# Kernel optimization log

Measured on AMD Instinct MI355X. Metric: run time of the kernel, lower is better.

## Reference

```python
import jax, jax.numpy as jnp
import numpy as np
from functools import partial

B, T, C, L, H, V = 2, 1024, 1024, 4, 16, 50257
HD = C // H
EPS = 1e-5


def setup_inputs() -> dict:
    key = jax.random.key(0)
    ks = jax.random.split(key, 12)
    s = 0.02
    inp = {
        'idx': jax.random.randint(ks[0], (B, T), 0, V),
        'wte': jax.random.normal(ks[1], (V, C), jnp.float32) * s,
        'wpe': jax.random.normal(ks[2], (T, C), jnp.float32) * s,
        'ln1_w': jnp.ones((L, C), jnp.float32),
        'ln1_b': jnp.zeros((L, C), jnp.float32),
        'attn_w': jax.random.normal(ks[3], (L, 3 * C, C), jnp.float32) * s,
        'attn_b': jnp.zeros((L, 3 * C), jnp.float32),
        'proj_w': jax.random.normal(ks[4], (L, C, C), jnp.float32) * s,
        'proj_b': jnp.zeros((L, C), jnp.float32),
        'ln2_w': jnp.ones((L, C), jnp.float32),
        'ln2_b': jnp.zeros((L, C), jnp.float32),
        'fc_w': jax.random.normal(ks[5], (L, 4 * C, C), jnp.float32) * s,
        'fc_b': jnp.zeros((L, 4 * C), jnp.float32),
        'fc2_w': jax.random.normal(ks[6], (L, C, 4 * C), jnp.float32) * s,
        'fc2_b': jnp.zeros((L, C), jnp.float32),
        'lnf_w': jnp.ones((C,), jnp.float32),
        'lnf_b': jnp.zeros((C,), jnp.float32),
    }
    return inp


def layer_norm(x, w, b):
    m = jnp.mean(x, axis=-1, keepdims=True)
    v = jnp.mean(jnp.square(x - m), axis=-1, keepdims=True)
    return (x - m) * jax.lax.rsqrt(v + EPS) * w + b


def block(x, p):
    (l1w, l1b, aw, ab, pw, pb, l2w, l2b, fw, fb, f2w, f2b) = p
    h = layer_norm(x, l1w, l1b)
    qkv = h @ aw.T + ab  # [B,T,3C]
    q, k, v = jnp.split(qkv, 3, axis=-1)
    q = q.reshape(B, T, H, HD).transpose(0, 2, 1, 3)
    k = k.reshape(B, T, H, HD).transpose(0, 2, 1, 3)
    v = v.reshape(B, T, H, HD).transpose(0, 2, 1, 3)
    # NOTE: source calls masked_fill without assignment -> causal mask is a
    # no-op; faithful reference uses UNMASKED full attention.
    scores = jnp.einsum('bhqd,bhkd->bhqk', q, k) / np.sqrt(HD).astype(np.float32)
    att = jax.nn.softmax(scores, axis=-1)
    o = jnp.einsum('bhqk,bhkd->bhqd', att, v)
    o = o.transpose(0, 2, 1, 3).reshape(B, T, C)
    x = x + (o @ pw.T + pb)
    h2 = layer_norm(x, l2w, l2b)
    h2 = jax.nn.gelu(h2 @ fw.T + fb, approximate=False)
    x = x + (h2 @ f2w.T + f2b)
    return x


def reference(idx, wte, wpe, ln1_w, ln1_b, attn_w, attn_b, proj_w, proj_b,
              ln2_w, ln2_b, fc_w, fc_b, fc2_w, fc2_b, lnf_w, lnf_b):
    x = wte[idx] + wpe[jnp.arange(T)][None, :, :]  # [B,T,C]
    params = (ln1_w, ln1_b, attn_w, attn_b, proj_w, proj_b,
              ln2_w, ln2_b, fc_w, fc_b, fc2_w, fc2_b)
    x, _ = jax.lax.scan(lambda c, p: (block(c, p), None), x, params)
    x = layer_norm(x, lnf_w, lnf_b)
    logits_last = x[:, -1] @ wte.T  # tied lm_head, only last position
    return logits_last
```

## Files before the change

kernel.cpp:

```cpp
#include <hip/hip_runtime.h>
#include <hip/hip_bf16.h>


constexpr int NB = 2;
constexpr int NT = 1024;
constexpr int NC = 1024;
constexpr int NLAYER = 4;
constexpr int NH = 16;
constexpr int DH = 64;
constexpr int NV = 50257;
constexpr int C3 = 3 * NC;
constexpr int C4 = 4 * NC;

typedef __attribute__((ext_vector_type(8))) short bf16x8;
typedef __attribute__((ext_vector_type(4))) float f32x4;
typedef __attribute__((ext_vector_type(4))) short s16x4;

__device__ inline short f2b(float x) {
  union { __hip_bfloat16 h; short s; } u;
  u.h = __float2bfloat16(x);
  return u.s;
}

__device__ inline bf16x8 cvt8(float4 a, float4 b) {
  bf16x8 r;
  r[0] = f2b(a.x); r[1] = f2b(a.y); r[2] = f2b(a.z); r[3] = f2b(a.w);
  r[4] = f2b(b.x); r[5] = f2b(b.y); r[6] = f2b(b.z); r[7] = f2b(b.w);
  return r;
}

__device__ inline void load_lds16(const short* gp, short* lp) {
  __builtin_amdgcn_global_load_lds(
      (const __attribute__((address_space(1))) void*)gp,
      (__attribute__((address_space(3))) void*)lp, 16, 0, 0);
}

__global__ __launch_bounds__(256) void cvt4_kernel(
    const float* __restrict__ s0, const float* __restrict__ s1,
    const float* __restrict__ s2, const float* __restrict__ s3,
    short* __restrict__ d0, short* __restrict__ d1,
    short* __restrict__ d2, short* __restrict__ d3,
    int n0, int n1, int n2, int n3) {
  int total = n0 + n1 + n2 + n3;
  int stride = gridDim.x * 256;
  for (int i = blockIdx.x * 256 + threadIdx.x; i < total; i += stride) {
    const float* s; short* d; int j = i;
    if (j < n0) { s = s0; d = d0; }
    else if ((j -= n0) < n1) { s = s1; d = d1; }
    else if ((j -= n1) < n2) { s = s2; d = d2; }
    else { j -= n2; s = s3; d = d3; }
    float4 v = reinterpret_cast<const float4*>(s)[j];
    s16x4 o;
    o[0] = f2b(v.x); o[1] = f2b(v.y); o[2] = f2b(v.z); o[3] = f2b(v.w);
    reinterpret_cast<s16x4*>(d)[j] = o;
  }
}

__global__ void embed_kernel(const int* __restrict__ idx,
                             const float* __restrict__ wte,
                             const float* __restrict__ wpe,
                             float* __restrict__ x) {
  int row = blockIdx.x;
  int t = row & (NT - 1);
  int id = idx[row];
  const float4* wr = reinterpret_cast<const float4*>(wte + (size_t)id * NC);
  const float4* pr = reinterpret_cast<const float4*>(wpe + (size_t)t * NC);
  float4* xr = reinterpret_cast<float4*>(x + (size_t)row * NC);
  int i = threadIdx.x;
  float4 a = wr[i], b = pr[i];
  xr[i] = make_float4(a.x + b.x, a.y + b.y, a.z + b.z, a.w + b.w);
}

__global__ __launch_bounds__(256) void ln_kernel(const float* __restrict__ x,
                                                 const float* __restrict__ w,
                                                 const float* __restrict__ bb,
                                                 short* __restrict__ out) {
  int wave = threadIdx.x >> 6;
  int lane = threadIdx.x & 63;
  int row = blockIdx.x * 4 + wave;
  const float4* xr = reinterpret_cast<const float4*>(x + (size_t)row * NC);
  float4 v[4];
  float s = 0.f;
#pragma unroll
  for (int i = 0; i < 4; i++) {
    v[i] = xr[lane + i * 64];
    s += v[i].x + v[i].y + v[i].z + v[i].w;
  }
#pragma unroll
  for (int m = 32; m; m >>= 1) s += __shfl_xor(s, m);
  float mean = s * (1.f / NC);
  float vs = 0.f;
#pragma unroll
  for (int i = 0; i < 4; i++) {
    float a = v[i].x - mean, b = v[i].y - mean, c = v[i].z - mean, d = v[i].w - mean;
    vs += a * a + b * b + c * c + d * d;
  }
#pragma unroll
  for (int m = 32; m; m >>= 1) vs += __shfl_xor(vs, m);
  float rstd = rsqrtf(vs * (1.f / NC) + 1e-5f);
  const float4* wr = reinterpret_cast<const float4*>(w);
  const float4* br = reinterpret_cast<const float4*>(bb);
  s16x4* orow = reinterpret_cast<s16x4*>(out + (size_t)row * NC);
#pragma unroll
  for (int i = 0; i < 4; i++) {
    int ci = lane + i * 64;
    float4 wv = wr[ci], bv = br[ci];
    s16x4 o;
    o[0] = f2b((v[i].x - mean) * rstd * wv.x + bv.x);
    o[1] = f2b((v[i].y - mean) * rstd * wv.y + bv.y);
    o[2] = f2b((v[i].z - mean) * rstd * wv.z + bv.z);
    o[3] = f2b((v[i].w - mean) * rstd * wv.w + bv.w);
    orow[ci] = o;
  }
}

template <int BM, int BN, int BK, int EPI>
__global__ __launch_bounds__(256) void gemm_kernel(
    const short* __restrict__ A, const short* __restrict__ Wb,
    const float* __restrict__ bias, float* __restrict__ outF,
    short* __restrict__ outB, short* __restrict__ vT, int N, int K) {
  constexpr int WM = BM / 2, WN = BN / 2;
  constexpr int FM = WM / 16, FN = WN / 16;
  constexpr int KS = BK / 32;
  constexpr int CA = BM * BK / 8;
  constexpr int CB = BN * BK / 8;
  constexpr int CT = CA + CB;
  constexpr int CPA = CA / KS;
  constexpr int CPB = CB / KS;
  static_assert(CA % 256 == 0 && CT % 256 == 0, "wave-uniform staging");
  __shared__ short As[BM * BK];
  __shared__ short Bs[BN * BK];
  int tid = threadIdx.x;
  int lane = tid & 63;
  int wave = tid >> 6;
  int quad = lane >> 4, l16 = lane & 15;
  int wm = (wave >> 1) * WM;
  int wn = (wave & 1) * WN;

  int nwg = gridDim.x * gridDim.y;
  int lin = blockIdx.y * gridDim.x + blockIdx.x;
  int swz = (lin & 7) * (nwg >> 3) + (lin >> 3);
  int bx = swz % gridDim.x;
  int by = swz / gridDim.x;

  const short* Ab = A + (size_t)(by * BM) * K;
  const short* Bb = Wb + (size_t)(bx * BN) * K;

  f32x4 acc[FM][FN] = {};
  for (int k0 = 0; k0 < K; k0 += BK) {
#pragma unroll
    for (int u = 0; u < CT / 256; u++) {
      int c = tid + u * 256;
      if (c < CA) {
        int ks = c / CPA, rem = c % CPA;
        int row = rem >> 2, kc = (rem & 3) * 8;
        load_lds16(Ab + (size_t)row * K + k0 + ks * 32 + kc, As + c * 8);
      } else {
        int c2 = c - CA;
        int ks = c2 / CPB, rem = c2 % CPB;
        int row = rem >> 2, kc = (rem & 3) * 8;
        load_lds16(Bb + (size_t)row * K + k0 + ks * 32 + kc, Bs + c2 * 8);
      }
    }
    __syncthreads();
#pragma unroll
    for (int s = 0; s < KS; s++) {
      bf16x8 a[FM], b[FN];
#pragma unroll
      for (int i = 0; i < FM; i++)
        a[i] = *reinterpret_cast<const bf16x8*>(As + s * BM * 32 + (wm + i * 16 + l16) * 32 + quad * 8);
#pragma unroll
      for (int j = 0; j < FN; j++)
        b[j] = *reinterpret_cast<const bf16x8*>(Bs + s * BN * 32 + (wn + j * 16 + l16) * 32 + quad * 8);
#pragma unroll
      for (int i = 0; i < FM; i++)
#pragma unroll
        for (int j = 0; j < FN; j++)
          acc[i][j] = __builtin_amdgcn_mfma_f32_16x16x32_bf16(a[i], b[j], acc[i][j], 0, 0, 0);
    }
    __syncthreads();
  }
#pragma unroll
  for (int j = 0; j < FN; j++) {
    int col = bx * BN + wn + j * 16 + l16;
    float bv = bias[col];
#pragma unroll
    for (int i = 0; i < FM; i++) {
#pragma unroll
      for (int r = 0; r < 4; r++) {
        int row = by * BM + wm + i * 16 + quad * 4 + r;
        float vv = acc[i][j][r] + bv;
        size_t off = (size_t)row * N + col;
        if constexpr (EPI == 0) {
          short sv = f2b(vv);
          outB[off] = sv;
          if (col >= 2 * NC) {
            int cg = col - 2 * NC;
            int hh = cg >> 6, d = cg & 63;
            int b = row >> 10, t = row & (NT - 1);
            vT[(size_t)(((b << 4) | hh) * DH + d) * NT + t] = sv;
          }
        } else if constexpr (EPI == 1) {
          outF[off] += vv;
        } else {
          float g = 0.5f * vv * (1.f + erff(vv * 0.70710678f));
          outB[off] = f2b(g);
        }
      }
    }
  }
}

__global__ __launch_bounds__(256) void attn_kernel(const short* __restrict__ qkv,
                                                   const short* __restrict__ vT,
                                                   short* __restrict__ o) {
  __shared__ __attribute__((aligned(16))) float Pl[4][16][36];
  int wave = threadIdx.x >> 6, lane = threadIdx.x & 63;
  int quad = lane >> 4, l16 = lane & 15;
  int bh = blockIdx.x >> 4;
  int qchunk = blockIdx.x & 15;
  int b = bh >> 4, h = bh & 15;
  int q0 = qchunk * 64 + wave * 16;

  bf16x8 aq[2];
#pragma unroll
  for (int kk = 0; kk < 2; kk++) {
    const short* qp = qkv + (size_t)(b * NT + q0 + l16) * C3 + h * DH + kk * 32 + quad * 8;
    aq[kk] = *reinterpret_cast<const bf16x8*>(qp);
  }
  f32x4 oacc[4] = {};
  float lr[4] = {0.f, 0.f, 0.f, 0.f};

  for (int t0 = 0; t0 < NT; t0 += 32) {
    f32x4 s0 = {}, s1 = {};
#pragma unroll
    for (int kk = 0; kk < 2; kk++) {
      const short* kp0 = qkv + (size_t)(b * NT + t0 + l16) * C3 + NC + h * DH + kk * 32 + quad * 8;
      bf16x8 bk0 = *reinterpret_cast<const bf16x8*>(kp0);
      bf16x8 bk1 = *reinterpret_cast<const bf16x8*>(kp0 + (size_t)16 * C3);
      s0 = __builtin_amdgcn_mfma_f32_16x16x32_bf16(aq[kk], bk0, s0, 0, 0, 0);
      s1 = __builtin_amdgcn_mfma_f32_16x16x32_bf16(aq[kk], bk1, s1, 0, 0, 0);
    }
    float p0[4], p1[4];
#pragma unroll
    for (int r = 0; r < 4; r++) {
      p0[r] = __expf(s0[r] * 0.125f);
      p1[r] = __expf(s1[r] * 0.125f);
      lr[r] += p0[r] + p1[r];
    }
#pragma unroll
    for (int r = 0; r < 4; r++) {
      Pl[wave][quad * 4 + r][l16] = p0[r];
      Pl[wave][quad * 4 + r][16 + l16] = p1[r];
    }
    asm volatile("" ::: "memory");
    float4 pv0 = *reinterpret_cast<const float4*>(&Pl[wave][l16][quad * 8]);
    float4 pv1 = *reinterpret_cast<const float4*>(&Pl[wave][l16][quad * 8 + 4]);
    asm volatile("" ::: "memory");
    bf16x8 pa = cvt8(pv0, pv1);
#pragma unroll
    for (int dt = 0; dt < 4; dt++) {
      const short* vp = vT + (size_t)(bh * DH + dt * 16 + l16) * NT + t0 + quad * 8;
      bf16x8 bv = *reinterpret_cast<const bf16x8*>(vp);
      oacc[dt] = __builtin_amdgcn_mfma_f32_16x16x32_bf16(pa, bv, oacc[dt], 0, 0, 0);
    }
  }
#pragma unroll
  for (int m = 1; m < 16; m <<= 1)
#pragma unroll
    for (int r = 0; r < 4; r++) lr[r] += __shfl_xor(lr[r], m);
  float inv[4];
#pragma unroll
  for (int r = 0; r < 4; r++) inv[r] = 1.f / lr[r];
#pragma unroll
  for (int dt = 0; dt < 4; dt++)
#pragma unroll
    for (int r = 0; r < 4; r++) {
      int row = q0 + quad * 4 + r;
      o[(size_t)(b * NT + row) * NC + h * DH + dt * 16 + l16] = f2b(oacc[dt][r] * inv[r]);
    }
}

__global__ __launch_bounds__(256) void lmhead_kernel(const float* __restrict__ x,
                                                     const float* __restrict__ lnf_w,
                                                     const float* __restrict__ lnf_b,
                                                     const float* __restrict__ wte,
                                                     float* __restrict__ out) {
  __shared__ float xs[2 * NC];
  int wave = threadIdx.x >> 6, lane = threadIdx.x & 63;
  if (wave < 2) {
    size_t row = (size_t)wave * NT + (NT - 1);
    const float4* xr = reinterpret_cast<const float4*>(x + row * NC);
    float4 v[4];
    float s = 0.f;
#pragma unroll
    for (int i = 0; i < 4; i++) {
      v[i] = xr[lane + i * 64];
      s += v[i].x + v[i].y + v[i].z + v[i].w;
    }
#pragma unroll
    for (int m = 32; m; m >>= 1) s += __shfl_xor(s, m);
    float mean = s * (1.f / NC);
    float vs = 0.f;
#pragma unroll
    for (int i = 0; i < 4; i++) {
      float a = v[i].x - mean, b = v[i].y - mean, c = v[i].z - mean, d = v[i].w - mean;
      vs += a * a + b * b + c * c + d * d;
    }
#pragma unroll
    for (int m = 32; m; m >>= 1) vs += __shfl_xor(vs, m);
    float rstd = rsqrtf(vs * (1.f / NC) + 1e-5f);
    const float4* wr = reinterpret_cast<const float4*>(lnf_w);
    const float4* br = reinterpret_cast<const float4*>(lnf_b);
#pragma unroll
    for (int i = 0; i < 4; i++) {
      int ci = lane + i * 64;
      float4 wv = wr[ci], bv = br[ci];
      float4 o;
      o.x = (v[i].x - mean) * rstd * wv.x + bv.x;
      o.y = (v[i].y - mean) * rstd * wv.y + bv.y;
      o.z = (v[i].z - mean) * rstd * wv.z + bv.z;
      o.w = (v[i].w - mean) * rstd * wv.w + bv.w;
      reinterpret_cast<float4*>(xs + wave * NC)[ci] = o;
    }
  }
  __syncthreads();
  int wglobal = blockIdx.x * 4 + wave;
  int stride = gridDim.x * 4;
  for (int v = wglobal; v < NV; v += stride) {
    const float4* wr = reinterpret_cast<const float4*>(wte + (size_t)v * NC);
    float a0 = 0.f, a1 = 0.f;
#pragma unroll
    for (int i = 0; i < 4; i++) {
      int ci = lane + i * 64;
      float4 wv = wr[ci];
      float4 x0 = reinterpret_cast<const float4*>(xs)[ci];
      float4 x1 = reinterpret_cast<const float4*>(xs + NC)[ci];
      a0 += wv.x * x0.x + wv.y * x0.y + wv.z * x0.z + wv.w * x0.w;
      a1 += wv.x * x1.x + wv.y * x1.y + wv.z * x1.z + wv.w * x1.w;
    }
#pragma unroll
    for (int m = 32; m; m >>= 1) {
      a0 += __shfl_xor(a0, m);
      a1 += __shfl_xor(a1, m);
    }
    if (lane == 0) {
      out[v] = a0;
      out[NV + v] = a1;
    }
  }
}

extern "C" void kernel_launch(void* const* d_in, const int* in_sizes, int n_in,
                              void* d_out, int out_size, void* d_ws, size_t ws_size,
                              hipStream_t stream) {
  const int* idx = (const int*)d_in[0];
  const float* wte = (const float*)d_in[1];
  const float* wpe = (const float*)d_in[2];
  const float* ln1_w = (const float*)d_in[3];
  const float* ln1_b = (const float*)d_in[4];
  const float* attn_w = (const float*)d_in[5];
  const float* attn_b = (const float*)d_in[6];
  const float* proj_w = (const float*)d_in[7];
  const float* proj_b = (const float*)d_in[8];
  const float* ln2_w = (const float*)d_in[9];
  const float* ln2_b = (const float*)d_in[10];
  const float* fc_w = (const float*)d_in[11];
  const float* fc_b = (const float*)d_in[12];
  const float* fc2_w = (const float*)d_in[13];
  const float* fc2_b = (const float*)d_in[14];
  const float* lnf_w = (const float*)d_in[15];
  const float* lnf_b = (const float*)d_in[16];

  char* ws = (char*)d_ws;
  size_t off = 0;
  float* x = (float*)(ws + off);  off += (size_t)NB * NT * NC * 4;
  short* h = (short*)(ws + off);  off += (size_t)NB * NT * NC * 2;
  short* qkv = (short*)(ws + off); off += (size_t)NB * NT * C3 * 2;
  short* vT = (short*)(ws + off); off += (size_t)NB * NH * DH * NT * 2;
  short* o = (short*)(ws + off);  off += (size_t)NB * NT * NC * 2;
  short* h2 = (short*)(ws + off); off += (size_t)NB * NT * C4 * 2;
  short* wb_attn = (short*)(ws + off); off += (size_t)NLAYER * C3 * NC * 2;
  short* wb_proj = (short*)(ws + off); off += (size_t)NLAYER * NC * NC * 2;
  short* wb_fc = (short*)(ws + off);   off += (size_t)NLAYER * C4 * NC * 2;
  short* wb_fc2 = (short*)(ws + off);  off += (size_t)NLAYER * NC * C4 * 2;

  cvt4_kernel<<<2048, 256, 0, stream>>>(
      attn_w, proj_w, fc_w, fc2_w, wb_attn, wb_proj, wb_fc, wb_fc2,
      NLAYER * C3 * NC / 4, NLAYER * NC * NC / 4,
      NLAYER * C4 * NC / 4, NLAYER * NC * C4 / 4);

  embed_kernel<<<NB * NT, 256, 0, stream>>>(idx, wte, wpe, x);

  for (int l = 0; l < NLAYER; l++) {
    ln_kernel<<<512, 256, 0, stream>>>(x, ln1_w + (size_t)l * NC, ln1_b + (size_t)l * NC, h);
    gemm_kernel<128, 128, 64, 0><<<dim3(C3 / 128, 16), 256, 0, stream>>>(
        h, wb_attn + (size_t)l * C3 * NC, attn_b + (size_t)l * C3, nullptr, qkv, vT, C3, NC);
    attn_kernel<<<512, 256, 0, stream>>>(qkv, vT, o);
    gemm_kernel<64, 64, 128, 1><<<dim3(NC / 64, 32), 256, 0, stream>>>(
        o, wb_proj + (size_t)l * NC * NC, proj_b + (size_t)l * NC, x, nullptr, nullptr, NC, NC);
    ln_kernel<<<512, 256, 0, stream>>>(x, ln2_w + (size_t)l * NC, ln2_b + (size_t)l * NC, h);
    gemm_kernel<128, 128, 64, 2><<<dim3(C4 / 128, 16), 256, 0, stream>>>(
        h, wb_fc + (size_t)l * C4 * NC, fc_b + (size_t)l * C4, nullptr, h2, nullptr, C4, NC);
    gemm_kernel<64, 64, 128, 1><<<dim3(NC / 64, 32), 256, 0, stream>>>(
        h2, wb_fc2 + (size_t)l * NC * C4, fc2_b + (size_t)l * NC, x, nullptr, nullptr, NC, C4);
  }

  lmhead_kernel<<<512, 256, 0, stream>>>(x, lnf_w, lnf_b, wte, (float*)d_out);
}
```

Measured before the change: 1.196 ms.

## Split attention key dimension across blocks and combine partial sums

Splits the attention key loop into four chunks handled by separate blocks via a second grid dimension. Each block writes unnormalized fp32 partial outputs and row sums, and a new combine kernel adds them and normalizes to bf16. This raises parallelism from 512 blocks so the GPU's CUs are better filled. The cost is extra fp32 partial-output traffic (about 32MB per layer) and an additional kernel launch. It stays correct because the softmax has no max subtraction, so partial sums combine by plain addition.

New measurement: 1.272 ms. +6.4%, slower.

```diff
diff --git a/kernel.cpp b/kernel.cpp
--- a/kernel.cpp
+++ b/kernel.cpp
@@ -11,6 +11,7 @@
 constexpr int NV = 50257;
 constexpr int C3 = 3 * NC;
 constexpr int C4 = 4 * NC;
+constexpr int ZSPLIT = 4;
 
 typedef __attribute__((ext_vector_type(8))) short bf16x8;
 typedef __attribute__((ext_vector_type(4))) float f32x4;
@@ -213,7 +214,8 @@
 
 __global__ __launch_bounds__(256) void attn_kernel(const short* __restrict__ qkv,
                                                    const short* __restrict__ vT,
-                                                   short* __restrict__ o) {
+                                                   float* __restrict__ oPart,
+                                                   float* __restrict__ lPart) {
   __shared__ __attribute__((aligned(16))) float Pl[4][16][36];
   int wave = threadIdx.x >> 6, lane = threadIdx.x & 63;
   int quad = lane >> 4, l16 = lane & 15;
@@ -221,6 +223,8 @@
   int qchunk = blockIdx.x & 15;
   int b = bh >> 4, h = bh & 15;
   int q0 = qchunk * 64 + wave * 16;
+  int z = blockIdx.y;
+  int tb = z * (NT / ZSPLIT), te = tb + NT / ZSPLIT;
 
   bf16x8 aq[2];
 #pragma unroll
@@ -231,7 +235,7 @@
   f32x4 oacc[4] = {};
   float lr[4] = {0.f, 0.f, 0.f, 0.f};
 
-  for (int t0 = 0; t0 < NT; t0 += 32) {
+  for (int t0 = tb; t0 < te; t0 += 32) {
     f32x4 s0 = {}, s1 = {};
 #pragma unroll
     for (int kk = 0; kk < 2; kk++) {
@@ -269,16 +273,43 @@
   for (int m = 1; m < 16; m <<= 1)
 #pragma unroll
     for (int r = 0; r < 4; r++) lr[r] += __shfl_xor(lr[r], m);
-  float inv[4];
-#pragma unroll
-  for (int r = 0; r < 4; r++) inv[r] = 1.f / lr[r];
+  float* oPr = oPart + (size_t)z * NB * NT * NC;
 #pragma unroll
   for (int dt = 0; dt < 4; dt++)
 #pragma unroll
     for (int r = 0; r < 4; r++) {
       int row = q0 + quad * 4 + r;
-      o[(size_t)(b * NT + row) * NC + h * DH + dt * 16 + l16] = f2b(oacc[dt][r] * inv[r]);
-    }
+      oPr[(size_t)(b * NT + row) * NC + h * DH + dt * 16 + l16] = oacc[dt][r];
+    }
+  if (l16 == 0) {
+#pragma unroll
+    for (int r = 0; r < 4; r++)
+      lPart[(size_t)z * NB * NH * NT + (size_t)bh * NT + q0 + quad * 4 + r] = lr[r];
+  }
+}
+
+__global__ __launch_bounds__(256) void attn_combine_kernel(
+    const float* __restrict__ oPart, const float* __restrict__ lPart,
+    short* __restrict__ o) {
+  int row = blockIdx.x;
+  int b = row >> 10, t = row & (NT - 1);
+  int i = threadIdx.x;
+  int h = i >> 4;
+  float l = 0.f;
+#pragma unroll
+  for (int zz = 0; zz < ZSPLIT; zz++)
+    l += lPart[(size_t)zz * NB * NH * NT + (size_t)(b * NH + h) * NT + t];
+  float4 s = make_float4(0.f, 0.f, 0.f, 0.f);
+#pragma unroll
+  for (int zz = 0; zz < ZSPLIT; zz++) {
+    float4 v = reinterpret_cast<const float4*>(oPart + (size_t)zz * NB * NT * NC + (size_t)row * NC)[i];
+    s.x += v.x; s.y += v.y; s.z += v.z; s.w += v.w;
+  }
+  float inv = 1.f / l;
+  s16x4 ov;
+  ov[0] = f2b(s.x * inv); ov[1] = f2b(s.y * inv);
+  ov[2] = f2b(s.z * inv); ov[3] = f2b(s.w * inv);
+  reinterpret_cast<s16x4*>(o + (size_t)row * NC)[i] = ov;
 }
 
 __global__ __launch_bounds__(256) void lmhead_kernel(const float* __restrict__ x,
@@ -380,6 +411,8 @@
   short* vT = (short*)(ws + off); off += (size_t)NB * NH * DH * NT * 2;
   short* o = (short*)(ws + off);  off += (size_t)NB * NT * NC * 2;
   short* h2 = (short*)(ws + off); off += (size_t)NB * NT * C4 * 2;
+  float* oPart = (float*)(ws + off); off += (size_t)ZSPLIT * NB * NT * NC * 4;
+  float* lPart = (float*)(ws + off); off += (size_t)ZSPLIT * NB * NH * NT * 4;
   short* wb_attn = (short*)(ws + off); off += (size_t)NLAYER * C3 * NC * 2;
   short* wb_proj = (short*)(ws + off); off += (size_t)NLAYER * NC * NC * 2;
   short* wb_fc = (short*)(ws + off);   off += (size_t)NLAYER * C4 * NC * 2;
@@ -396,7 +429,8 @@
     ln_kernel<<<512, 256, 0, stream>>>(x, ln1_w + (size_t)l * NC, ln1_b + (size_t)l * NC, h);
     gemm_kernel<128, 128, 64, 0><<<dim3(C3 / 128, 16), 256, 0, stream>>>(
         h, wb_attn + (size_t)l * C3 * NC, attn_b + (size_t)l * C3, nullptr, qkv, vT, C3, NC);
-    attn_kernel<<<512, 256, 0, stream>>>(qkv, vT, o);
+    attn_kernel<<<dim3(512, ZSPLIT), 256, 0, stream>>>(qkv, vT, oPart, lPart);
+    attn_combine_kernel<<<NB * NT, 256, 0, stream>>>(oPart, lPart, o);
     gemm_kernel<64, 64, 128, 1><<<dim3(NC / 64, 32), 256, 0, stream>>>(
         o, wb_proj + (size_t)l * NC * NC, proj_b + (size_t)l * NC, x, nullptr, nullptr, NC, NC);
     ln_kernel<<<512, 256, 0, stream>>>(x, ln2_w + (size_t)l * NC, ln2_b + (size_t)l * NC, h);
```
